# Performance work log

Measured on AMD Instinct MI355X. Metric: run time of the kernel, lower is better.

Reference implementation:

```python
import jax, jax.numpy as jnp
import numpy as np

B, N, M, NUM_CLASSES = 32, 16384, 128, 81
NUM_LOGITS = 5 + NUM_CLASSES - 6  # pred[:, 6:]
SMALL_OBJ_AREA_THR = 0.01
SMALL_OBJ_WEIGHT = 1.5
NEG = -1e9


def setup_inputs() -> dict:
    key = jax.random.key(0)
    k1, k2, k3, k4 = jax.random.split(key, 4)
    preds = jax.random.uniform(k1, (B, N, 5 + NUM_CLASSES), dtype=jnp.float32)
    coords = jax.random.uniform(k2, (B, M, 4), dtype=jnp.float32)
    cls = jax.random.randint(k3, (B, M), 0, NUM_LOGITS).astype(jnp.float32)
    keep = jax.random.uniform(k4, (B, M)) < 0.6
    cls = jnp.where(keep, cls, -1.0)
    targets = jnp.concatenate([coords, cls[..., None]], axis=-1)
    return {"preds": preds, "targets": targets}


def _smooth_l1(x, y):
    d = x - y
    ad = jnp.abs(d)
    return jnp.where(ad < 1.0, 0.5 * d * d, ad - 0.5)


def _bce(p, t):
    # matches torch F.binary_cross_entropy's log clamp at -100
    lp = jnp.maximum(jnp.log(p), -100.0)
    ln = jnp.maximum(jnp.log1p(-p), -100.0)
    return -(t * lp + (1.0 - t) * ln)


def _per_image(pred, target):
    pred_boxes = pred[:, :4]            # [N,4]
    conf = pred[:, 4]                   # [N]
    logits = pred[:, 6:]                # [N, NUM_LOGITS]
    tb = target[:, :4]                  # [M,4]
    valid = target[:, 4] != -1.0        # [M]

    # pairwise IoU [N, M]
    x1 = jnp.maximum(pred_boxes[:, None, 0], tb[None, :, 0])
    y1 = jnp.maximum(pred_boxes[:, None, 1], tb[None, :, 1])
    x2 = jnp.minimum(pred_boxes[:, None, 2], tb[None, :, 2])
    y2 = jnp.minimum(pred_boxes[:, None, 3], tb[None, :, 3])
    inter = jnp.clip(x2 - x1, 0.0) * jnp.clip(y2 - y1, 0.0)
    area1 = (pred_boxes[:, 2] - pred_boxes[:, 0]) * (pred_boxes[:, 3] - pred_boxes[:, 1])
    area2 = (tb[:, 2] - tb[:, 0]) * (tb[:, 3] - tb[:, 1])
    iou = inter / (area1[:, None] + area2[None, :] - inter + 1e-6)
    iou = jnp.where(valid[None, :], iou, NEG)  # mask padded targets out of the max

    best_iou = iou.max(axis=1)          # [N]
    best_idx = iou.argmax(axis=1)       # [N] (first max, like torch)

    matched = best_iou > 0.4
    matched = jnp.where(matched.any(), matched, best_iou == best_iou.max())
    mf = matched.astype(pred.dtype)
    n_m = mf.sum()
    n_m_safe = jnp.maximum(n_m, 1.0)

    g_tb = tb[best_idx]                 # [N,4] matched target boxes
    areas = (g_tb[:, 2] - g_tb[:, 0]) * (g_tb[:, 3] - g_tb[:, 1])
    w = jnp.where(areas < SMALL_OBJ_AREA_THR, SMALL_OBJ_WEIGHT, 1.0)
    bbox = _smooth_l1(pred_boxes, g_tb) * w[:, None]       # [N,4]
    bbox_loss = (bbox * mf[:, None]).sum() / (n_m_safe * 4.0)

    logp = jax.nn.log_softmax(logits, axis=-1)
    cls_idx = jnp.clip(target[best_idx, 4].astype(jnp.int32), 0, NUM_LOGITS - 1)
    nll = -jnp.take_along_axis(logp, cls_idx[:, None], axis=1)[:, 0]
    cls_loss = (nll * mf).sum() / n_m_safe

    m_conf = (_bce(conf, 1.0) * mf).sum() / n_m_safe
    n_u = jnp.asarray(N, pred.dtype) - n_m
    u_conf = (_bce(conf, 0.0) * (1.0 - mf)).sum() / jnp.maximum(n_u, 1.0)
    conf_loss = jnp.where(n_u > 0, (m_conf + u_conf) / 2.0, m_conf)

    full = bbox_loss * 5.0 + cls_loss * 1.0 + conf_loss * 2.0
    empty = _bce(conf, 0.0).mean()
    return jnp.where(valid.any(), full, empty)


def reference(preds, targets):
    per_image = jax.vmap(_per_image)(preds, targets)  # [B]
    return per_image.mean()
```

## Files before the change

kernel.cpp:

```cpp
#include <hip/hip_runtime.h>
#include <math.h>

namespace {

constexpr int B_ = 32;
constexpr int N_ = 16384;
constexpr int M_ = 128;
constexpr int NLOG_ = 80;
constexpr int ROW_ = 86;
constexpr float NEG_ = -1000000000.0f;
constexpr int TPB = 256;
constexpr int RPT = 4;
constexpr int BPI = N_ / (TPB * RPT);
constexpr int BLOCKS = B_ * BPI;
constexpr int RSTR = 16;
constexpr int NW = TPB / 64;

__device__ inline float sl1(float d) {
  float ad = fabsf(d);
  return (ad < 1.0f) ? 0.5f * d * d : ad - 0.5f;
}

__global__ __launch_bounds__(TPB, 4) void k_main(const float* __restrict__ preds,
                                                 const float* __restrict__ targets,
                                                 float* __restrict__ recs) {
  const int b = blockIdx.x / BPI;
  const int blk = blockIdx.x % BPI;
  const int t = threadIdx.x;
  const int lane = t & 63, wid = t >> 6;

  __shared__ float traw[M_ * 5];
  __shared__ float4 sbox[M_];
  __shared__ float sa2e[M_];
  __shared__ float sw_[M_];
  __shared__ float scl[M_];
  __shared__ int scnt2[2];
  __shared__ float smax[NW];
  __shared__ float wacc[NW][12];

  const float* tg = targets + (size_t)b * M_ * 5;
  float tva = tg[t];
  float tvb = tg[t + 256];
  float tvc = (t < 128) ? tg[t + 512] : 0.f;

  const float* pb = preds + (size_t)b * N_ * ROW_;
  const int r0 = blk * (TPB * RPT) + t;
  float2 h01[RPT], h23[RPT];
#pragma unroll
  for (int rr = 0; rr < RPT; rr++) {
    const float* p = pb + (size_t)(r0 + rr * TPB) * ROW_;
    h01[rr] = *(const float2*)(p);
    h23[rr] = *(const float2*)(p + 2);
  }

  traw[t] = tva;
  traw[t + 256] = tvb;
  if (t < 128) traw[t + 512] = tvc;
  __syncthreads();

  float bx1 = 0, by1 = 0, bx2 = 0, by2 = 0, bcl = 0;
  bool tvalid = false;
  int tpos = 0;
  if (t < M_) {
    bx1 = traw[t * 5 + 0]; by1 = traw[t * 5 + 1];
    bx2 = traw[t * 5 + 2]; by2 = traw[t * 5 + 3];
    bcl = traw[t * 5 + 4];
    tvalid = (bcl != -1.0f);
    unsigned long long ball = __ballot(tvalid);
    if (lane == 0) scnt2[wid] = __popcll(ball);
    tpos = __popcll(ball & ((1ull << lane) - 1ull));
  }
  __syncthreads();
  const int nv = scnt2[0] + scnt2[1];
  const int nvp = (nv + 3) & ~3;
  if (t < M_) {
    if (tvalid) {
      int pos = tpos + (wid ? scnt2[0] : 0);
      sbox[pos] = make_float4(bx1, by1, bx2, by2);
      float ra = (bx2 - bx1) * (by2 - by1);
      sa2e[pos] = ra + 1e-6f;
      sw_[pos] = (ra < 0.01f) ? 1.5f : 1.0f;
      scl[pos] = bcl;
    }
    if (t >= nv && t < nvp) {
      sbox[t] = make_float4(0.f, 0.f, 0.f, 0.f);
      sa2e[t] = __int_as_float(0x7fc00000);
      sw_[t] = 1.0f;
      scl[t] = 0.f;
    }
  }
  __syncthreads();

  float a1[RPT], best[RPT];
  int bj[RPT];
#pragma unroll
  for (int rr = 0; rr < RPT; rr++) {
    a1[rr] = (h23[rr].x - h01[rr].x) * (h23[rr].y - h01[rr].y);
    best[rr] = NEG_;
    bj[rr] = 0;
  }
  for (int j = 0; j < nvp; j += 4) {
    float4 tb[4] = {sbox[j], sbox[j + 1], sbox[j + 2], sbox[j + 3]};
    float4 aev = *(const float4*)(&sa2e[j]);
    float ae[4] = {aev.x, aev.y, aev.z, aev.w};
#pragma unroll
    for (int jj = 0; jj < 4; jj++) {
#pragma unroll
      for (int rr = 0; rr < RPT; rr++) {
        float x1 = fmaxf(h01[rr].x, tb[jj].x);
        float y1 = fmaxf(h01[rr].y, tb[jj].y);
        float x2 = fminf(h23[rr].x, tb[jj].z);
        float y2 = fminf(h23[rr].y, tb[jj].w);
        float inter = fmaxf(x2 - x1, 0.f) * fmaxf(y2 - y1, 0.f);
        float u = (a1[rr] + ae[jj]) - inter;
        float iou = inter * __builtin_amdgcn_rcpf(u);
        bool gt = iou > best[rr];
        best[rr] = gt ? iou : best[rr];
        bj[rr] = gt ? (j + jj) : bj[rr];
      }
    }
  }

  float hc[RPT];
#pragma unroll
  for (int rr = 0; rr < RPT; rr++) {
    hc[rr] = pb[(size_t)(r0 + rr * TPB) * ROW_ + 4];
  }

  float mx = fmaxf(fmaxf(best[0], best[1]), fmaxf(best[2], best[3]));
#pragma unroll
  for (int off = 32; off; off >>= 1) mx = fmaxf(mx, __shfl_xor(mx, off));
  if (lane == 0) smax[wid] = mx;
  __syncthreads();
  float blockmax = smax[0];
#pragma unroll
  for (int w = 1; w < NW; w++) blockmax = fmaxf(blockmax, smax[w]);

  float v[11] = {0, 0, 0, 0, 0, 0, 0, 0, 0, 0, 0};
#pragma unroll
  for (int rr = 0; rr < RPT; rr++) {
    float conf = hc[rr];
    float bce0 = -fmaxf(__logf(1.0f - conf), -100.0f);
    v[5] += bce0;
    bool mA = (nv > 0) && (best[rr] > 0.4f);
    bool mB = (nv > 0) && (best[rr] == blockmax);
    if (mA || mB) {
      int g = bj[rr];
      float4 gb = sbox[g];
      float w_ = sw_[g];
      int ci = (int)scl[g];
      ci = ci < 0 ? 0 : (ci > NLOG_ - 1 ? NLOG_ - 1 : ci);
      float sb = w_ * (sl1(h01[rr].x - gb.x) + sl1(h01[rr].y - gb.y) +
                       sl1(h23[rr].x - gb.z) + sl1(h23[rr].y - gb.w));
      float bce1 = -fmaxf(__logf(conf), -100.0f);
      const float* p = pb + (size_t)(r0 + rr * TPB) * ROW_;
      const float2* l2 = (const float2*)(p + 6);
      float se = 0.f;
#pragma unroll 10
      for (int k = 0; k < NLOG_ / 2; k++) {
        float2 lv = l2[k];
        se += __expf(lv.x) + __expf(lv.y);
      }
      float nll = __logf(se) - p[6 + ci];
      if (mA) { v[0] += 1.f; v[1] += sb; v[2] += nll; v[3] += bce1; v[4] += bce0; }
      if (mB) { v[6] += 1.f; v[7] += sb; v[8] += nll; v[9] += bce1; v[10] += bce0; }
    }
  }

#pragma unroll
  for (int i = 0; i < 11; i++) {
    float x = v[i];
#pragma unroll
    for (int off = 32; off; off >>= 1) x += __shfl_xor(x, off);
    if (lane == 0) wacc[wid][i] = x;
  }
  __syncthreads();
  float* rec = recs + (size_t)blockIdx.x * RSTR;
  if (t < 11) {
    float s = 0.f;
#pragma unroll
    for (int w = 0; w < NW; w++) s += wacc[w][t];
    rec[1 + t] = s;
  }
  if (t == 12) rec[0] = blockmax;
  if (t == 13) rec[12] = (float)nv;
}

__global__ __launch_bounds__(256) void k_final(const float* __restrict__ recs,
                                               float* __restrict__ out) {
  const int t = threadIdx.x;
  const int b = t >> 3, g = t & 7;
  __shared__ float limg[B_];

  const float* rb = recs + (size_t)b * BPI * RSTR;
  float aA[6] = {0, 0, 0, 0, 0, 0};
  float bmax = NEG_;
#pragma unroll
  for (int q = 0; q < BPI / 8; q++) {
    const float* r = rb + (size_t)(g + 8 * q) * RSTR;
    bmax = fmaxf(bmax, r[0]);
#pragma unroll
    for (int i = 0; i < 5; i++) aA[i] += r[1 + i];
    aA[5] += r[6];
  }
#pragma unroll
  for (int off = 1; off < 8; off <<= 1) {
    bmax = fmaxf(bmax, __shfl_xor(bmax, off));
#pragma unroll
    for (int i = 0; i < 6; i++) aA[i] += __shfl_xor(aA[i], off);
  }
  float aB[5] = {0, 0, 0, 0, 0};
#pragma unroll
  for (int q = 0; q < BPI / 8; q++) {
    const float* r = rb + (size_t)(g + 8 * q) * RSTR;
    if (r[0] == bmax) {
#pragma unroll
      for (int i = 0; i < 5; i++) aB[i] += r[7 + i];
    }
  }
#pragma unroll
  for (int off = 1; off < 8; off <<= 1) {
#pragma unroll
    for (int i = 0; i < 5; i++) aB[i] += __shfl_xor(aB[i], off);
  }

  if (g == 0) {
    float nv = rb[12];
    float b0all = aA[5];
    float loss;
    if (nv == 0.f) {
      loss = b0all * (1.0f / (float)N_);
    } else {
      float nm, bbox, nll, bce1, bce0m;
      if (aA[0] > 0.f) {
        nm = aA[0]; bbox = aA[1]; nll = aA[2]; bce1 = aA[3]; bce0m = aA[4];
      } else {
        nm = aB[0]; bbox = aB[1]; nll = aB[2]; bce1 = aB[3]; bce0m = aB[4];
      }
      float nms = fmaxf(nm, 1.0f);
      float bbox_loss = bbox / (nms * 4.0f);
      float cls_loss = nll / nms;
      float m_conf = bce1 / nms;
      float n_u = (float)N_ - nm;
      float u_conf = (b0all - bce0m) / fmaxf(n_u, 1.0f);
      float conf_loss = (n_u > 0.f) ? 0.5f * (m_conf + u_conf) : m_conf;
      loss = 5.0f * bbox_loss + cls_loss + 2.0f * conf_loss;
    }
    limg[b] = loss;
  }
  __syncthreads();
  if (t < 32) {
    float x = limg[t];
#pragma unroll
    for (int off = 1; off < 32; off <<= 1) x += __shfl_xor(x, off);
    if (t == 0) out[0] = x * (1.0f / (float)B_);
  }
}

}

extern "C" void kernel_launch(void* const* d_in, const int* in_sizes, int n_in,
                              void* d_out, int out_size, void* d_ws, size_t ws_size,
                              hipStream_t stream) {
  const float* preds = (const float*)d_in[0];
  const float* targets = (const float*)d_in[1];
  float* recs = (float*)d_ws;

  k_main<<<dim3(BLOCKS), dim3(TPB), 0, stream>>>(preds, targets, recs);
  k_final<<<dim3(1), dim3(256), 0, stream>>>(recs, (float*)d_out);
}
```

Measured before the change: 49.95 us.

## Fuse final reduction into main kernel via last-block counter, halve rows per thread

```diff
diff --git a/kernel.cpp b/kernel.cpp
--- a/kernel.cpp
+++ b/kernel.cpp
@@ -10,12 +10,14 @@
 constexpr int ROW_ = 86;
 constexpr float NEG_ = -1000000000.0f;
 constexpr int TPB = 256;
-constexpr int RPT = 4;
+constexpr int RPT = 2;
 constexpr int BPI = N_ / (TPB * RPT);
 constexpr int BLOCKS = B_ * BPI;
 constexpr int RSTR = 16;
 constexpr int NW = TPB / 64;
 
+typedef float vf2 __attribute__((ext_vector_type(2)));
+
 __device__ inline float sl1(float d) {
   float ad = fabsf(d);
   return (ad < 1.0f) ? 0.5f * d * d : ad - 0.5f;
@@ -23,7 +25,9 @@
 
 __global__ __launch_bounds__(TPB, 4) void k_main(const float* __restrict__ preds,
                                                  const float* __restrict__ targets,
-                                                 float* __restrict__ recs) {
+                                                 float* __restrict__ recs,
+                                                 unsigned* __restrict__ counter,
+                                                 float* __restrict__ out) {
   const int b = blockIdx.x / BPI;
   const int blk = blockIdx.x % BPI;
   const int t = threadIdx.x;
@@ -37,6 +41,8 @@
   __shared__ int scnt2[2];
   __shared__ float smax[NW];
   __shared__ float wacc[NW][12];
+  __shared__ int s_last;
+  __shared__ float limg[B_];
 
   const float* tg = targets + (size_t)b * M_ * 5;
   float tva = tg[t];
@@ -45,12 +51,14 @@
 
   const float* pb = preds + (size_t)b * N_ * ROW_;
   const int r0 = blk * (TPB * RPT) + t;
-  float2 h01[RPT], h23[RPT];
+  vf2 h01[RPT], h23[RPT];
+  float hc[RPT];
 #pragma unroll
   for (int rr = 0; rr < RPT; rr++) {
     const float* p = pb + (size_t)(r0 + rr * TPB) * ROW_;
-    h01[rr] = *(const float2*)(p);
-    h23[rr] = *(const float2*)(p + 2);
+    h01[rr] = __builtin_nontemporal_load((const vf2*)(p));
+    h23[rr] = __builtin_nontemporal_load((const vf2*)(p + 2));
+    hc[rr] = __builtin_nontemporal_load(p + 4);
   }
 
   traw[t] = tva;
@@ -121,13 +129,7 @@
     }
   }
 
-  float hc[RPT];
-#pragma unroll
-  for (int rr = 0; rr < RPT; rr++) {
-    hc[rr] = pb[(size_t)(r0 + rr * TPB) * ROW_ + 4];
-  }
-
-  float mx = fmaxf(fmaxf(best[0], best[1]), fmaxf(best[2], best[3]));
+  float mx = fmaxf(best[0], best[RPT - 1]);
 #pragma unroll
   for (int off = 32; off; off >>= 1) mx = fmaxf(mx, __shfl_xor(mx, off));
   if (lane == 0) smax[wid] = mx;
@@ -154,14 +156,14 @@
                        sl1(h23[rr].x - gb.z) + sl1(h23[rr].y - gb.w));
       float bce1 = -fmaxf(__logf(conf), -100.0f);
       const float* p = pb + (size_t)(r0 + rr * TPB) * ROW_;
-      const float2* l2 = (const float2*)(p + 6);
+      const vf2* l2 = (const vf2*)(p + 6);
       float se = 0.f;
 #pragma unroll 10
       for (int k = 0; k < NLOG_ / 2; k++) {
-        float2 lv = l2[k];
+        vf2 lv = __builtin_nontemporal_load(&l2[k]);
         se += __expf(lv.x) + __expf(lv.y);
       }
-      float nll = __logf(se) - p[6 + ci];
+      float nll = __logf(se) - __builtin_nontemporal_load(p + 6 + ci);
       if (mA) { v[0] += 1.f; v[1] += sb; v[2] += nll; v[3] += bce1; v[4] += bce0; }
       if (mB) { v[6] += 1.f; v[7] += sb; v[8] += nll; v[9] += bce1; v[10] += bce0; }
     }
@@ -184,69 +186,74 @@
   }
   if (t == 12) rec[0] = blockmax;
   if (t == 13) rec[12] = (float)nv;
-}
-
-__global__ __launch_bounds__(256) void k_final(const float* __restrict__ recs,
-                                               float* __restrict__ out) {
-  const int t = threadIdx.x;
-  const int b = t >> 3, g = t & 7;
-  __shared__ float limg[B_];
-
-  const float* rb = recs + (size_t)b * BPI * RSTR;
-  float aA[6] = {0, 0, 0, 0, 0, 0};
-  float bmax = NEG_;
-#pragma unroll
-  for (int q = 0; q < BPI / 8; q++) {
-    const float* r = rb + (size_t)(g + 8 * q) * RSTR;
-    bmax = fmaxf(bmax, r[0]);
-#pragma unroll
-    for (int i = 0; i < 5; i++) aA[i] += r[1 + i];
-    aA[5] += r[6];
-  }
-#pragma unroll
-  for (int off = 1; off < 8; off <<= 1) {
-    bmax = fmaxf(bmax, __shfl_xor(bmax, off));
-#pragma unroll
-    for (int i = 0; i < 6; i++) aA[i] += __shfl_xor(aA[i], off);
-  }
-  float aB[5] = {0, 0, 0, 0, 0};
-#pragma unroll
-  for (int q = 0; q < BPI / 8; q++) {
-    const float* r = rb + (size_t)(g + 8 * q) * RSTR;
-    if (r[0] == bmax) {
-#pragma unroll
-      for (int i = 0; i < 5; i++) aB[i] += r[7 + i];
-    }
-  }
-#pragma unroll
-  for (int off = 1; off < 8; off <<= 1) {
-#pragma unroll
-    for (int i = 0; i < 5; i++) aB[i] += __shfl_xor(aB[i], off);
-  }
-
-  if (g == 0) {
-    float nv = rb[12];
-    float b0all = aA[5];
-    float loss;
-    if (nv == 0.f) {
-      loss = b0all * (1.0f / (float)N_);
-    } else {
-      float nm, bbox, nll, bce1, bce0m;
-      if (aA[0] > 0.f) {
-        nm = aA[0]; bbox = aA[1]; nll = aA[2]; bce1 = aA[3]; bce0m = aA[4];
+  __syncthreads();
+
+  if (t == 0) {
+    __threadfence();
+    unsigned tk = atomicAdd(counter, 1u);
+    s_last = ((tk & (unsigned)(BLOCKS - 1)) == (unsigned)(BLOCKS - 1)) ? 1 : 0;
+  }
+  __syncthreads();
+  if (!s_last) return;
+  __threadfence();
+
+  {
+    const int im = t >> 3, g = t & 7;
+    const float* rb = recs + (size_t)im * BPI * RSTR;
+    float aA[6] = {0, 0, 0, 0, 0, 0};
+    float bmax = NEG_;
+#pragma unroll
+    for (int q = 0; q < BPI / 8; q++) {
+      const float* r = rb + (size_t)(g + 8 * q) * RSTR;
+      bmax = fmaxf(bmax, r[0]);
+#pragma unroll
+      for (int i = 0; i < 5; i++) aA[i] += r[1 + i];
+      aA[5] += r[6];
+    }
+#pragma unroll
+    for (int off = 1; off < 8; off <<= 1) {
+      bmax = fmaxf(bmax, __shfl_xor(bmax, off));
+#pragma unroll
+      for (int i = 0; i < 6; i++) aA[i] += __shfl_xor(aA[i], off);
+    }
+    float aB[5] = {0, 0, 0, 0, 0};
+#pragma unroll
+    for (int q = 0; q < BPI / 8; q++) {
+      const float* r = rb + (size_t)(g + 8 * q) * RSTR;
+      if (r[0] == bmax) {
+#pragma unroll
+        for (int i = 0; i < 5; i++) aB[i] += r[7 + i];
+      }
+    }
+#pragma unroll
+    for (int off = 1; off < 8; off <<= 1) {
+#pragma unroll
+      for (int i = 0; i < 5; i++) aB[i] += __shfl_xor(aB[i], off);
+    }
+    if (g == 0) {
+      float nvf = rb[12];
+      float b0all = aA[5];
+      float loss;
+      if (nvf == 0.f) {
+        loss = b0all * (1.0f / (float)N_);
       } else {
-        nm = aB[0]; bbox = aB[1]; nll = aB[2]; bce1 = aB[3]; bce0m = aB[4];
-      }
-      float nms = fmaxf(nm, 1.0f);
-      float bbox_loss = bbox / (nms * 4.0f);
-      float cls_loss = nll / nms;
-      float m_conf = bce1 / nms;
-      float n_u = (float)N_ - nm;
-      float u_conf = (b0all - bce0m) / fmaxf(n_u, 1.0f);
-      float conf_loss = (n_u > 0.f) ? 0.5f * (m_conf + u_conf) : m_conf;
-      loss = 5.0f * bbox_loss + cls_loss + 2.0f * conf_loss;
-    }
-    limg[b] = loss;
+        float nm, bbox, nll, bce1, bce0m;
+        if (aA[0] > 0.f) {
+          nm = aA[0]; bbox = aA[1]; nll = aA[2]; bce1 = aA[3]; bce0m = aA[4];
+        } else {
+          nm = aB[0]; bbox = aB[1]; nll = aB[2]; bce1 = aB[3]; bce0m = aB[4];
+        }
+        float nms = fmaxf(nm, 1.0f);
+        float bbox_loss = bbox / (nms * 4.0f);
+        float cls_loss = nll / nms;
+        float m_conf = bce1 / nms;
+        float n_u = (float)N_ - nm;
+        float u_conf = (b0all - bce0m) / fmaxf(n_u, 1.0f);
+        float conf_loss = (n_u > 0.f) ? 0.5f * (m_conf + u_conf) : m_conf;
+        loss = 5.0f * bbox_loss + cls_loss + 2.0f * conf_loss;
+      }
+      limg[im] = loss;
+    }
   }
   __syncthreads();
   if (t < 32) {
@@ -264,8 +271,11 @@
                               hipStream_t stream) {
   const float* preds = (const float*)d_in[0];
   const float* targets = (const float*)d_in[1];
-  float* recs = (float*)d_ws;
-
-  k_main<<<dim3(BLOCKS), dim3(TPB), 0, stream>>>(preds, targets, recs);
-  k_final<<<dim3(1), dim3(256), 0, stream>>>(recs, (float*)d_out);
-}
+
+  char* ws = (char*)d_ws;
+  float* recs = (float*)ws;
+  unsigned* counter = (unsigned*)(ws + 65536);
+
+  k_main<<<dim3(BLOCKS), dim3(TPB), 0, stream>>>(preds, targets, recs, counter,
+                                                 (float*)d_out);
+}
```

Result: slower. 64.53 us (+29.2%).
